# Optimization experiments

Hardware: AMD Instinct MI355X
Metric: run time of the kernel (lower is better)

The kernel has to match this reference:

```python
import jax, jax.numpy as jnp
import numpy as np


def setup_inputs() -> dict:
    key = jax.random.key(0)
    k1, k2 = jax.random.split(key)
    B, T, F = 8, 1000, 257
    m = jax.random.normal(k1, (B, 27, T, F), dtype=jnp.float32)
    x = jax.random.normal(k2, (B, F, T, 2), dtype=jnp.float32)
    v = jnp.array([[1.0, -0.5, -0.5], [0.0, np.sqrt(3) / 2, -np.sqrt(3) / 2]], dtype=jnp.float32)
    return {"m": m, "x": x, "v": v}


def reference(m, x, v):
    B, C, T, F = m.shape
    # m -> (B, 3, 9, T, F); contract the complex-basis dim (3) with v rows
    m5 = m.reshape(B, 3, C // 3, T, F)
    H_real = jnp.einsum('k,bkntf->bntf', v[0], m5)  # (B, 9, T, F)
    H_imag = jnp.einsum('k,bkntf->bntf', v[1], m5)
    M_real = H_real.reshape(B, 3, 3, T, F)
    M_imag = H_imag.reshape(B, 3, 3, T, F)

    # x: (B,F,T,2) -> (B,2,T,F), pad: time causal (top=2), freq symmetric (1,1)
    xp = jnp.transpose(x, (0, 3, 2, 1))
    xp = jnp.pad(xp, ((0, 0), (0, 0), (2, 0), (1, 1)))
    # 3x3 unfold as 9 shifted views: (B, 2, 3, 3, T, F)
    xu = jnp.stack(
        [xp[:, :, i:i + T, j:j + F] for i in range(3) for j in range(3)],
        axis=2,
    ).reshape(B, 2, 3, 3, T, F)

    xr, xi = xu[:, 0], xu[:, 1]
    x_enh_real = jnp.sum(M_real * xr - M_imag * xi, axis=(1, 2))  # (B, T, F)
    x_enh_imag = jnp.sum(M_real * xi + M_imag * xr, axis=(1, 2))
    x_enh = jnp.stack([x_enh_real, x_enh_imag], axis=3)  # (B, T, F, 2)
    return jnp.transpose(x_enh, (0, 2, 1, 3))  # (B, F, T, 2)
```

## Files before the change

### kernel.cpp

```cpp
#include <hip/hip_runtime.h>


constexpr int B = 8, C = 27, T = 1000, F = 257;
constexpr int TCH = 4;
constexpr int NT  = T / TCH;
constexpr int BLK = 320;
constexpr int NA  = 257;
constexpr int TROW = TCH + 2;
constexpr int FP   = 260;
constexpr int PLSZ = TROW * FP + 32;
constexpr size_t CS = (size_t)T * F;

__device__ __forceinline__ int XSW(int a) { return a ^ (((a >> 5) & 7) << 2); }
__device__ __forceinline__ float comp(const float4& v, int r) {
    return r == 0 ? v.x : (r == 1 ? v.y : (r == 2 ? v.z : v.w));
}

__global__ __launch_bounds__(BLK, 3)
void ccm_kernel(const float* __restrict__ m,
                const float* __restrict__ x,
                float* __restrict__ out) {
    __shared__ float xs[2 * PLSZ];

    const int bid = blockIdx.x;
    const int tc  = bid % NT;
    const int b   = bid / NT;
    const int t0  = tc * TCH;
    const int tx  = threadIdx.x;

    const float* xb = x + (size_t)b * F * T * 2;

    if (tx < 259) {
        const int f = tx - 1;
        float vre[6], vim[6];
        #pragma unroll
        for (int tt = 0; tt < 6; ++tt) { vre[tt] = 0.f; vim[tt] = 0.f; }
        if (f >= 0 && f < F) {
            if (t0 >= 2) {
                const float4* src = reinterpret_cast<const float4*>(
                    xb + ((size_t)f * T + (t0 - 2)) * 2);
                const float4 p0 = src[0], p1 = src[1], p2 = src[2];
                vre[0] = p0.x; vim[0] = p0.y; vre[1] = p0.z; vim[1] = p0.w;
                vre[2] = p1.x; vim[2] = p1.y; vre[3] = p1.z; vim[3] = p1.w;
                vre[4] = p2.x; vim[4] = p2.y; vre[5] = p2.z; vim[5] = p2.w;
            } else {
                #pragma unroll
                for (int tt = 0; tt < 6; ++tt) {
                    const int t = t0 - 2 + tt;
                    if (t >= 0) {
                        const float2 v2 = *reinterpret_cast<const float2*>(
                            xb + ((size_t)f * T + t) * 2);
                        vre[tt] = v2.x; vim[tt] = v2.y;
                    }
                }
            }
        }
        #pragma unroll
        for (int tt = 0; tt < 6; ++tt) {
            const int a = XSW(tt * FP + tx);
            xs[a]        = vre[tt];
            xs[PLSZ + a] = vim[tt];
        }
    }
    __syncthreads();

    if (tx >= NA) return;

    const int e0 = 4 * tx;
    const int tl = e0 / 257;
    const int f0 = e0 - tl * 257;

    const float SQ3_2 = 0.8660254037844386f;
    const float* mseg = m + (size_t)b * C * CS + (size_t)t0 * F + 4 * tx;

    float4 g[9][3];
#define LOADG(n)                                                            \
    {                                                                       \
        g[n][0] = *reinterpret_cast<const float4*>(mseg + (size_t)(n) * CS);       \
        g[n][1] = *reinterpret_cast<const float4*>(mseg + (size_t)((n) + 9) * CS); \
        g[n][2] = *reinterpret_cast<const float4*>(mseg + (size_t)((n) + 18) * CS);\
    }

#define MAC_N(n, WRE, WIE)                                                  \
    {                                                                       \
        constexpr int i_ = (n) / 3, j_ = (n) % 3;                           \
        _Pragma("unroll")                                                   \
        for (int r = 0; r < 4; ++r) {                                       \
            const float a0 = comp(g[n][0], r);                              \
            const float a1 = comp(g[n][1], r);                              \
            const float a2 = comp(g[n][2], r);                              \
            const float hr = a0 - 0.5f * (a1 + a2);                         \
            const float hi = SQ3_2 * (a1 - a2);                             \
            accr[r] += hr * WRE(r, i_, j_) - hi * WIE(r, i_, j_);           \
            acci[r] += hr * WIE(r, i_, j_) + hi * WRE(r, i_, j_);           \
        }                                                                   \
    }

    float accr[4] = {0.f, 0.f, 0.f, 0.f};
    float acci[4] = {0.f, 0.f, 0.f, 0.f};

    LOADG(0); LOADG(1); LOADG(2);

    if (f0 <= 253) {
        float wr[3][6], wi[3][6];
        #pragma unroll
        for (int i = 0; i < 3; ++i) {
            const int rowb = (tl + i) * FP + f0;
            #pragma unroll
            for (int k = 0; k < 6; ++k) {
                const int a = XSW(rowb + k);
                wr[i][k] = xs[a];
                wi[i][k] = xs[PLSZ + a];
            }
        }
#define WF_R(r, i, j) wr[i][(r) + (j)]
#define WF_I(r, i, j) wi[i][(r) + (j)]
        LOADG(3); MAC_N(0, WF_R, WF_I);
        LOADG(4); MAC_N(1, WF_R, WF_I);
        LOADG(5); MAC_N(2, WF_R, WF_I);
        LOADG(6); MAC_N(3, WF_R, WF_I);
        LOADG(7); MAC_N(4, WF_R, WF_I);
        LOADG(8); MAC_N(5, WF_R, WF_I);
        MAC_N(6, WF_R, WF_I);
        MAC_N(7, WF_R, WF_I);
        MAC_N(8, WF_R, WF_I);
#undef WF_R
#undef WF_I
    } else {
        int tlr_[4], fr_[4];
        #pragma unroll
        for (int r = 0; r < 4; ++r) {
            const int w = (f0 + r) >= 257 ? 1 : 0;
            tlr_[r] = tl + w;
            fr_[r]  = f0 + r - 257 * w;
        }
#define WS_R(r, i, j) xs[XSW((tlr_[r] + (i)) * FP + fr_[r] + (j))]
#define WS_I(r, i, j) xs[PLSZ + XSW((tlr_[r] + (i)) * FP + fr_[r] + (j))]
        LOADG(3); MAC_N(0, WS_R, WS_I);
        LOADG(4); MAC_N(1, WS_R, WS_I);
        LOADG(5); MAC_N(2, WS_R, WS_I);
        LOADG(6); MAC_N(3, WS_R, WS_I);
        LOADG(7); MAC_N(4, WS_R, WS_I);
        LOADG(8); MAC_N(5, WS_R, WS_I);
        MAC_N(6, WS_R, WS_I);
        MAC_N(7, WS_R, WS_I);
        MAC_N(8, WS_R, WS_I);
#undef WS_R
#undef WS_I
    }
#undef LOADG
#undef MAC_N

    #pragma unroll
    for (int r = 0; r < 4; ++r) {
        const int w  = (f0 + r) >= 257 ? 1 : 0;
        const int fr = f0 + r - 257 * w;
        const int tr = t0 + tl + w;
        *reinterpret_cast<float2*>(out + ((size_t)(b * F + fr) * T + tr) * 2) =
            make_float2(accr[r], acci[r]);
    }
}

extern "C" void kernel_launch(void* const* d_in, const int* in_sizes, int n_in,
                              void* d_out, int out_size, void* d_ws, size_t ws_size,
                              hipStream_t stream) {
    const float* m = (const float*)d_in[0];
    const float* x = (const float*)d_in[1];
    float* out = (float*)d_out;

    const int grid = B * NT;
    ccm_kernel<<<grid, BLK, 0, stream>>>(m, x, out);
}
```

Measured before the change: 66.66 us.

## Stage outputs through LDS for coalesced stores and rotate m-load registers

Results are now written into shared memory (reusing the x tile buffer) and read back transposed, so each thread stores its frequency's four time steps as two contiguous float4 writes instead of scattered float2 writes. The m loads use a three-buffer rotation that keeps up to three taps of loads in flight ahead of the MACs, with fewer live registers than the old 9x3 array. The launch bound now targets 4 waves/blocks per CU. The price is two extra block barriers, and the tighter register budget could cause spills.

```diff
diff --git a/kernel.cpp b/kernel.cpp
--- a/kernel.cpp
+++ b/kernel.cpp
@@ -9,6 +9,7 @@
 constexpr int TROW = TCH + 2;
 constexpr int FP   = 260;
 constexpr int PLSZ = TROW * FP + 32;
+constexpr int LDSW = 2 * PLSZ;
 constexpr size_t CS = (size_t)T * F;
 
 __device__ __forceinline__ int XSW(int a) { return a ^ (((a >> 5) & 7) << 2); }
@@ -16,11 +17,11 @@
     return r == 0 ? v.x : (r == 1 ? v.y : (r == 2 ? v.z : v.w));
 }
 
-__global__ __launch_bounds__(BLK, 3)
+__global__ __launch_bounds__(BLK, 4)
 void ccm_kernel(const float* __restrict__ m,
                 const float* __restrict__ x,
                 float* __restrict__ out) {
-    __shared__ float xs[2 * PLSZ];
+    __shared__ float xs[LDSW];
 
     const int bid = blockIdx.x;
     const int tc  = bid % NT;
@@ -62,102 +63,109 @@
             xs[PLSZ + a] = vim[tt];
         }
     }
-    __syncthreads();
-
-    if (tx >= NA) return;
 
     const int e0 = 4 * tx;
     const int tl = e0 / 257;
     const int f0 = e0 - tl * 257;
+    const bool active = (tx < NA);
 
     const float SQ3_2 = 0.8660254037844386f;
     const float* mseg = m + (size_t)b * C * CS + (size_t)t0 * F + 4 * tx;
 
-    float4 g[9][3];
-#define LOADG(n)                                                            \
-    {                                                                       \
-        g[n][0] = *reinterpret_cast<const float4*>(mseg + (size_t)(n) * CS);       \
-        g[n][1] = *reinterpret_cast<const float4*>(mseg + (size_t)((n) + 9) * CS); \
-        g[n][2] = *reinterpret_cast<const float4*>(mseg + (size_t)((n) + 18) * CS);\
-    }
-
-#define MAC_N(n, WRE, WIE)                                                  \
-    {                                                                       \
-        constexpr int i_ = (n) / 3, j_ = (n) % 3;                           \
-        _Pragma("unroll")                                                   \
-        for (int r = 0; r < 4; ++r) {                                       \
-            const float a0 = comp(g[n][0], r);                              \
-            const float a1 = comp(g[n][1], r);                              \
-            const float a2 = comp(g[n][2], r);                              \
-            const float hr = a0 - 0.5f * (a1 + a2);                         \
-            const float hi = SQ3_2 * (a1 - a2);                             \
-            accr[r] += hr * WRE(r, i_, j_) - hi * WIE(r, i_, j_);           \
-            acci[r] += hr * WIE(r, i_, j_) + hi * WRE(r, i_, j_);           \
-        }                                                                   \
-    }
-
+    float4 ga[3], gb[3], gc[3];
     float accr[4] = {0.f, 0.f, 0.f, 0.f};
     float acci[4] = {0.f, 0.f, 0.f, 0.f};
 
-    LOADG(0); LOADG(1); LOADG(2);
+#define LOADG(Gv, n)                                                          \
+    {                                                                         \
+        Gv[0] = *reinterpret_cast<const float4*>(mseg + (size_t)(n) * CS);        \
+        Gv[1] = *reinterpret_cast<const float4*>(mseg + (size_t)((n) + 9) * CS);  \
+        Gv[2] = *reinterpret_cast<const float4*>(mseg + (size_t)((n) + 18) * CS); \
+    }
 
-    if (f0 <= 253) {
-        float wr[3][6], wi[3][6];
-        #pragma unroll
-        for (int i = 0; i < 3; ++i) {
-            const int rowb = (tl + i) * FP + f0;
+#define MACG(Gv, n, WRE, WIE)                                                 \
+    {                                                                         \
+        constexpr int i_ = (n) / 3, j_ = (n) % 3;                             \
+        _Pragma("unroll")                                                     \
+        for (int r = 0; r < 4; ++r) {                                         \
+            const float a0 = comp(Gv[0], r);                                  \
+            const float a1 = comp(Gv[1], r);                                  \
+            const float a2 = comp(Gv[2], r);                                  \
+            const float hr = a0 - 0.5f * (a1 + a2);                           \
+            const float hi = SQ3_2 * (a1 - a2);                               \
+            accr[r] += hr * WRE(r, i_, j_) - hi * WIE(r, i_, j_);             \
+            acci[r] += hr * WIE(r, i_, j_) + hi * WRE(r, i_, j_);             \
+        }                                                                     \
+    }
+
+#define SCHED(WRE, WIE)                                                       \
+    LOADG(ga, 0) LOADG(gb, 1) LOADG(gc, 2)                                    \
+    MACG(ga, 0, WRE, WIE) LOADG(ga, 3)                                        \
+    MACG(gb, 1, WRE, WIE) LOADG(gb, 4)                                        \
+    MACG(gc, 2, WRE, WIE) LOADG(gc, 5)                                        \
+    MACG(ga, 3, WRE, WIE) LOADG(ga, 6)                                        \
+    MACG(gb, 4, WRE, WIE) LOADG(gb, 7)                                        \
+    MACG(gc, 5, WRE, WIE) LOADG(gc, 8)                                        \
+    MACG(ga, 6, WRE, WIE) MACG(gb, 7, WRE, WIE) MACG(gc, 8, WRE, WIE)
+
+    __syncthreads();
+
+    int tlr_[4], fr_[4];
+    #pragma unroll
+    for (int r = 0; r < 4; ++r) {
+        const int w = (f0 + r) >= 257 ? 1 : 0;
+        tlr_[r] = tl + w;
+        fr_[r]  = f0 + r - 257 * w;
+    }
+
+    if (active) {
+        if (f0 <= 253) {
+            float wr[3][6], wi[3][6];
             #pragma unroll
-            for (int k = 0; k < 6; ++k) {
-                const int a = XSW(rowb + k);
-                wr[i][k] = xs[a];
-                wi[i][k] = xs[PLSZ + a];
+            for (int i = 0; i < 3; ++i) {
+                const int rowb = (tl + i) * FP + f0;
+                #pragma unroll
+                for (int k = 0; k < 6; ++k) {
+                    const int a = XSW(rowb + k);
+                    wr[i][k] = xs[a];
+                    wi[i][k] = xs[PLSZ + a];
+                }
             }
-        }
 #define WF_R(r, i, j) wr[i][(r) + (j)]
 #define WF_I(r, i, j) wi[i][(r) + (j)]
-        LOADG(3); MAC_N(0, WF_R, WF_I);
-        LOADG(4); MAC_N(1, WF_R, WF_I);
-        LOADG(5); MAC_N(2, WF_R, WF_I);
-        LOADG(6); MAC_N(3, WF_R, WF_I);
-        LOADG(7); MAC_N(4, WF_R, WF_I);
-        LOADG(8); MAC_N(5, WF_R, WF_I);
-        MAC_N(6, WF_R, WF_I);
-        MAC_N(7, WF_R, WF_I);
-        MAC_N(8, WF_R, WF_I);
+            SCHED(WF_R, WF_I)
 #undef WF_R
 #undef WF_I
-    } else {
-        int tlr_[4], fr_[4];
-        #pragma unroll
-        for (int r = 0; r < 4; ++r) {
-            const int w = (f0 + r) >= 257 ? 1 : 0;
-            tlr_[r] = tl + w;
-            fr_[r]  = f0 + r - 257 * w;
-        }
+        } else {
 #define WS_R(r, i, j) xs[XSW((tlr_[r] + (i)) * FP + fr_[r] + (j))]
 #define WS_I(r, i, j) xs[PLSZ + XSW((tlr_[r] + (i)) * FP + fr_[r] + (j))]
-        LOADG(3); MAC_N(0, WS_R, WS_I);
-        LOADG(4); MAC_N(1, WS_R, WS_I);
-        LOADG(5); MAC_N(2, WS_R, WS_I);
-        LOADG(6); MAC_N(3, WS_R, WS_I);
-        LOADG(7); MAC_N(4, WS_R, WS_I);
-        LOADG(8); MAC_N(5, WS_R, WS_I);
-        MAC_N(6, WS_R, WS_I);
-        MAC_N(7, WS_R, WS_I);
-        MAC_N(8, WS_R, WS_I);
+            SCHED(WS_R, WS_I)
 #undef WS_R
 #undef WS_I
+        }
     }
+#undef SCHED
 #undef LOADG
-#undef MAC_N
+#undef MACG
 
-    #pragma unroll
-    for (int r = 0; r < 4; ++r) {
-        const int w  = (f0 + r) >= 257 ? 1 : 0;
-        const int fr = f0 + r - 257 * w;
-        const int tr = t0 + tl + w;
-        *reinterpret_cast<float2*>(out + ((size_t)(b * F + fr) * T + tr) * 2) =
-            make_float2(accr[r], acci[r]);
+    __syncthreads();
+
+    if (active) {
+        float2* res = reinterpret_cast<float2*>(xs);
+        #pragma unroll
+        for (int r = 0; r < 4; ++r)
+            res[fr_[r] * 4 + tlr_[r]] = make_float2(accr[r], acci[r]);
+    }
+    __syncthreads();
+
+    if (tx < NA) {
+        const int f = tx;
+        const float4* res4 = reinterpret_cast<const float4*>(xs);
+        const float4 q0 = res4[f * 2];
+        const float4 q1 = res4[f * 2 + 1];
+        float* op = out + ((size_t)(b * F + f) * T + t0) * 2;
+        reinterpret_cast<float4*>(op)[0] = q0;
+        reinterpret_cast<float4*>(op)[1] = q1;
     }
 }
 
```

Result: slower. 69.34 us (+4.0%).
